# Kernel tuning notes

Hardware: AMD Instinct MI355X
Metric: run time of the kernel (lower is better)

Reference implementation:

```python
import jax, jax.numpy as jnp
import numpy as np

B, N, F, H = 256, 512, 256, 256
NUM_STAGES = 5
LN_EPS = 1e-5


def layer_norm(x, gamma, beta):
    m = jnp.mean(x, axis=-1, keepdims=True)
    v = jnp.mean((x - m) ** 2, axis=-1, keepdims=True)
    return (x - m) / jnp.sqrt(v + LN_EPS) * gamma + beta


def setup_inputs() -> dict:
    key = jax.random.key(0)
    ks = jax.random.split(key, 16)
    inp = {
        'adjacency': jax.random.normal(ks[0], (B, N, N), dtype=jnp.float32),
        'features': jax.random.normal(ks[1], (B, N, F), dtype=jnp.float32),
        'stage_ids': jax.random.randint(ks[2], (B, N), 0, NUM_STAGES, dtype=jnp.int32),
        # gc[0]: weight + bias
        'W0': jax.random.normal(ks[3], (F, H), dtype=jnp.float32) / np.sqrt(F),
        'b0': jax.random.normal(ks[4], (H,), dtype=jnp.float32) * 0.01,
        # gc[1]: bias only (weight=False)
        'b1': jax.random.normal(ks[5], (H,), dtype=jnp.float32) * 0.01,
        # gc[2]: weight + bias
        'W2': jax.random.normal(ks[6], (H, H), dtype=jnp.float32) / np.sqrt(H),
        'b2': jax.random.normal(ks[7], (H,), dtype=jnp.float32) * 0.01,
        # LayerNorm params (3 layers)
        'g0': jnp.ones((H,), jnp.float32), 'be0': jnp.zeros((H,), jnp.float32),
        'g1': jnp.ones((H,), jnp.float32), 'be1': jnp.zeros((H,), jnp.float32),
        'g2': jnp.ones((H,), jnp.float32), 'be2': jnp.zeros((H,), jnp.float32),
        # final fc: nhid -> 1
        'fcW': jax.random.normal(ks[8], (H, 1), dtype=jnp.float32) / np.sqrt(H),
        'fcb': jnp.zeros((1,), jnp.float32),
    }
    return inp


def reference(adjacency, features, stage_ids, W0, b0, b1, W2, b2,
              g0, be0, g1, be1, g2, be2, fcW, fcb):
    # --- layer 0: GraphConvolution(F->H) + LN + ReLU ---
    support = jnp.einsum('bnf,fh->bnh', features, W0)
    x = jnp.einsum('bnm,bmh->bnh', adjacency, support) + b0  # [B,N,H]
    x = jax.nn.relu(layer_norm(x, g0, be0))

    # --- layer 1: bias-add + ragged per-stage sum/argmax pooling ---
    out = x + b1                              # [B,N,H]
    scores = jnp.sum(out, axis=-1)            # [B,N] per-node row sums
    groups = jnp.arange(NUM_STAGES)
    in_group = stage_ids[:, None, :] == groups[None, :, None]  # [B,5,N]
    masked = jnp.where(in_group, scores[:, None, :], -jnp.inf)
    idx = jnp.argmax(masked, axis=-1)         # [B,5] best node per stage
    pooled = jnp.take_along_axis(out, idx[:, :, None], axis=1)  # [B,5,H]
    x = jax.nn.relu(layer_norm(pooled, g1, be1))

    # --- layer 2: GraphConvolution(H->H) with fixed 5x5 adjacency ---
    final_adj = jnp.zeros((NUM_STAGES, NUM_STAGES), x.dtype).at[0].set(1.0)
    support2 = jnp.einsum('bsh,hk->bsk', x, W2)
    x = jnp.einsum('ij,bjh->bih', final_adj, support2) + b2  # [B,5,H]
    x = jax.nn.relu(layer_norm(x, g2, be2))

    # --- head: fc(x[:, 0]) ---
    return x[:, 0] @ fcW + fcb                # [B,1]
```

## Files before the change

### kernel.cpp

```cpp
#include <hip/hip_runtime.h>
#include <stdint.h>

#define Bn 256
#define Nn 512
#define Fn 256
#define Hn 256
#define NSn 5
#define EPS 1e-5f
#define LSTR 56

typedef __attribute__((ext_vector_type(8))) short bf16x8;
typedef __attribute__((ext_vector_type(4))) float f32x4;

__device__ __forceinline__ unsigned short f2bf(float x) {
  unsigned int u = __float_as_uint(x);
  u += 0x7FFFu + ((u >> 16) & 1u);
  return (unsigned short)(u >> 16);
}
__device__ __forceinline__ unsigned int pack2bf(float a, float b) {
  return (unsigned int)f2bf(a) | ((unsigned int)f2bf(b) << 16);
}

__global__ __launch_bounds__(256) void k0_prep(const float* __restrict__ W0,
                                               unsigned short* __restrict__ W0T) {
  int idx = blockIdx.x * 256 + (int)threadIdx.x;
  int h = idx >> 8, f = idx & 255;
  W0T[h * Fn + f] = f2bf(W0[(size_t)f * Hn + h]);
}

__global__ __launch_bounds__(256) void k1_support(
    const float* __restrict__ feat, const unsigned short* __restrict__ W0T,
    unsigned short* __restrict__ supT)
{
  __shared__ __align__(16) unsigned short As[64 * LSTR];
  __shared__ __align__(16) unsigned short Bs[256 * LSTR];
  const int tid = (int)threadIdx.x;
  const int wv = tid >> 6, lane = tid & 63;
  const int m0 = blockIdx.x * 64;
  f32x4 acc[4][4];
  const f32x4 z4 = {0.f, 0.f, 0.f, 0.f};
#pragma unroll
  for (int i = 0; i < 4; ++i)
#pragma unroll
    for (int j = 0; j < 4; ++j) acc[i][j] = z4;

  const int ar = tid >> 2, ac = tid & 3;
  for (int k0 = 0; k0 < Fn; k0 += 32) {
    const float* ap = feat + (size_t)(m0 + ar) * Fn + k0 + ac * 4;
    float4 v0 = *(const float4*)ap;
    float4 v1 = *(const float4*)(ap + 16);
    *(uint2*)&As[ar * LSTR + ac * 4] =
        make_uint2(pack2bf(v0.x, v0.y), pack2bf(v0.z, v0.w));
    *(uint2*)&As[ar * LSTR + 16 + ac * 4] =
        make_uint2(pack2bf(v1.x, v1.y), pack2bf(v1.z, v1.w));
#pragma unroll
    for (int q = 0; q < 4; ++q) {
      int s = q * 256 + tid;
      int h = s >> 2, c = s & 3;
      *(uint4*)&Bs[h * LSTR + c * 8] =
          *(const uint4*)(W0T + (size_t)h * Fn + k0 + c * 8);
    }
    __syncthreads();
    bf16x8 af[4], bfr[4];
#pragma unroll
    for (int i = 0; i < 4; ++i) {
      af[i]  = *(const bf16x8*)&As[(i * 16 + (lane & 15)) * LSTR + (lane >> 4) * 8];
      bfr[i] = *(const bf16x8*)&Bs[(wv * 64 + i * 16 + (lane & 15)) * LSTR + (lane >> 4) * 8];
    }
#pragma unroll
    for (int mi = 0; mi < 4; ++mi)
#pragma unroll
      for (int nt = 0; nt < 4; ++nt)
        acc[mi][nt] = __builtin_amdgcn_mfma_f32_16x16x32_bf16(af[mi], bfr[nt], acc[mi][nt], 0, 0, 0);
    __syncthreads();
  }
  const int b = m0 >> 9;
  const int nodebase = m0 & 511;
  unsigned short* outb = supT + ((size_t)b << 17);
#pragma unroll
  for (int mi = 0; mi < 4; ++mi)
#pragma unroll
    for (int nt = 0; nt < 4; ++nt) {
      int h = wv * 64 + nt * 16 + (lane & 15);
      int node = nodebase + mi * 16 + (lane >> 4) * 4;
      *(uint2*)(outb + (size_t)h * Nn + node) =
          make_uint2(pack2bf(acc[mi][nt][0], acc[mi][nt][1]),
                     pack2bf(acc[mi][nt][2], acc[mi][nt][3]));
    }
}

__global__ __launch_bounds__(256) void k2_scores(
    const float* __restrict__ adj, const unsigned short* __restrict__ supT,
    const float* __restrict__ b0, const float* __restrict__ g0,
    const float* __restrict__ be0, float* __restrict__ scores)
{
  __shared__ __align__(16) unsigned short As[64 * LSTR];
  __shared__ __align__(16) unsigned short Bs[256 * LSTR];
  const int tid = (int)threadIdx.x;
  const int wv = tid >> 6, lane = tid & 63;
  const int b = blockIdx.x & 255;
  const int m0 = (blockIdx.x >> 8) * 64;
  const float* adjb = adj + ((size_t)b << 18);
  const unsigned short* supb = supT + ((size_t)b << 17);
  f32x4 acc[4][4];
  const f32x4 z4 = {0.f, 0.f, 0.f, 0.f};
#pragma unroll
  for (int i = 0; i < 4; ++i)
#pragma unroll
    for (int j = 0; j < 4; ++j) acc[i][j] = z4;

  const int ar = tid >> 2, ac = tid & 3;
  for (int k0 = 0; k0 < Nn; k0 += 32) {
    const float* ap = adjb + (size_t)(m0 + ar) * Nn + k0 + ac * 4;
    float4 v0 = *(const float4*)ap;
    float4 v1 = *(const float4*)(ap + 16);
    *(uint2*)&As[ar * LSTR + ac * 4] =
        make_uint2(pack2bf(v0.x, v0.y), pack2bf(v0.z, v0.w));
    *(uint2*)&As[ar * LSTR + 16 + ac * 4] =
        make_uint2(pack2bf(v1.x, v1.y), pack2bf(v1.z, v1.w));
#pragma unroll
    for (int q = 0; q < 4; ++q) {
      int s = q * 256 + tid;
      int h = s >> 2, c = s & 3;
      *(uint4*)&Bs[h * LSTR + c * 8] =
          *(const uint4*)(supb + (size_t)h * Nn + k0 + c * 8);
    }
    __syncthreads();
    bf16x8 af[4], bfr[4];
#pragma unroll
    for (int i = 0; i < 4; ++i) {
      af[i]  = *(const bf16x8*)&As[(i * 16 + (lane & 15)) * LSTR + (lane >> 4) * 8];
      bfr[i] = *(const bf16x8*)&Bs[(wv * 64 + i * 16 + (lane & 15)) * LSTR + (lane >> 4) * 8];
    }
#pragma unroll
    for (int mi = 0; mi < 4; ++mi)
#pragma unroll
      for (int nt = 0; nt < 4; ++nt)
        acc[mi][nt] = __builtin_amdgcn_mfma_f32_16x16x32_bf16(af[mi], bfr[nt], acc[mi][nt], 0, 0, 0);
    __syncthreads();
  }

  float* red = (float*)As;
  float b0v[4], g0v[4], be0v[4];
#pragma unroll
  for (int nt = 0; nt < 4; ++nt) {
    int col = wv * 64 + nt * 16 + (lane & 15);
    b0v[nt] = b0[col]; g0v[nt] = g0[col]; be0v[nt] = be0[col];
  }
#pragma unroll
  for (int mi = 0; mi < 4; ++mi)
#pragma unroll
    for (int rg = 0; rg < 4; ++rg) {
      float s1 = 0.f, s2 = 0.f;
#pragma unroll
      for (int nt = 0; nt < 4; ++nt) {
        float x = acc[mi][nt][rg] + b0v[nt];
        s1 += x; s2 += x * x;
      }
#pragma unroll
      for (int off = 8; off >= 1; off >>= 1) {
        s1 += __shfl_xor(s1, off);
        s2 += __shfl_xor(s2, off);
      }
      if ((lane & 15) == 0) {
        int row = mi * 16 + (lane >> 4) * 4 + rg;
        red[row * 4 + wv] = s1;
        red[256 + row * 4 + wv] = s2;
      }
    }
  __syncthreads();
#pragma unroll
  for (int mi = 0; mi < 4; ++mi)
#pragma unroll
    for (int rg = 0; rg < 4; ++rg) {
      int row = mi * 16 + (lane >> 4) * 4 + rg;
      float s1 = red[row*4] + red[row*4+1] + red[row*4+2] + red[row*4+3];
      float s2 = red[256+row*4] + red[256+row*4+1] + red[256+row*4+2] + red[256+row*4+3];
      float m = s1 * (1.0f / Hn);
      float var = s2 * (1.0f / Hn) - m * m;
      float rstd = 1.0f / sqrtf(var + EPS);
      float sc = 0.f;
#pragma unroll
      for (int nt = 0; nt < 4; ++nt) {
        float x = acc[mi][nt][rg] + b0v[nt];
        float zz = (x - m) * rstd * g0v[nt] + be0v[nt];
        sc += fmaxf(zz, 0.f);
      }
#pragma unroll
      for (int off = 8; off >= 1; off >>= 1) sc += __shfl_xor(sc, off);
      if ((lane & 15) == 0) red[512 + row * 4 + wv] = sc;
    }
  __syncthreads();
  if (tid < 64) {
    float s = red[512+tid*4] + red[512+tid*4+1] + red[512+tid*4+2] + red[512+tid*4+3];
    scores[b * Nn + m0 + tid] = s;
  }
}

__device__ __forceinline__ float brs(float v) {
  __shared__ float sb[4];
#pragma unroll
  for (int off = 32; off >= 1; off >>= 1) v += __shfl_xor(v, off);
  __syncthreads();
  if ((threadIdx.x & 63) == 0) sb[threadIdx.x >> 6] = v;
  __syncthreads();
  return sb[0] + sb[1] + sb[2] + sb[3];
}

__global__ __launch_bounds__(256) void k3_final(
    const float* __restrict__ adj, const float* __restrict__ feat,
    const float* __restrict__ scores, const int* __restrict__ sid,
    const float* __restrict__ W0, const float* __restrict__ b0,
    const float* __restrict__ b1, const float* __restrict__ W2,
    const float* __restrict__ b2, const float* __restrict__ g0,
    const float* __restrict__ be0, const float* __restrict__ g1,
    const float* __restrict__ be1, const float* __restrict__ g2,
    const float* __restrict__ be2, const float* __restrict__ fcW,
    const float* __restrict__ fcb, float* __restrict__ out)
{
  __shared__ float sc_s[Nn];
  __shared__ int sid_s[Nn];
  __shared__ __align__(16) float tT[Fn][20];
  __shared__ float xb[20][Hn];
  __shared__ unsigned long long redk[4];
  __shared__ int cand[20];
  __shared__ int candv[20];
  __shared__ float cm[20], cr[20], csc[20];
  __shared__ float xs[Hn];
  __shared__ int winslot[NSn];
  const int tid = (int)threadIdx.x;
  const int b = blockIdx.x;

  for (int i = tid; i < Nn; i += 256) {
    sc_s[i] = scores[b * Nn + i];
    sid_s[i] = sid[b * Nn + i];
  }
  __syncthreads();

  for (int s = 0; s < NSn; ++s) {
    for (int j = 0; j < 4; ++j) {
      unsigned long long best = 0ull;
      for (int i = tid; i < Nn; i += 256) {
        if (sid_s[i] == s) {
          unsigned int fbt = __float_as_uint(sc_s[i]);
          fbt = (fbt & 0x80000000u) ? ~fbt : (fbt | 0x80000000u);
          unsigned long long key = ((unsigned long long)fbt << 32) |
                                   (unsigned long long)(unsigned)(Nn - 1 - i);
          if (key > best) best = key;
        }
      }
#pragma unroll
      for (int off = 32; off >= 1; off >>= 1) {
        unsigned long long o = __shfl_xor(best, off);
        if (o > best) best = o;
      }
      __syncthreads();
      if ((tid & 63) == 0) redk[tid >> 6] = best;
      __syncthreads();
      best = redk[0];
      if (redk[1] > best) best = redk[1];
      if (redk[2] > best) best = redk[2];
      if (redk[3] > best) best = redk[3];
      if (tid == 0) {
        int c = s * 4 + j;
        if (best != 0ull) {
          int node = Nn - 1 - (int)(best & 0xFFFFFFFFull);
          cand[c] = node; candv[c] = 1; sid_s[node] = -1;
        } else {
          cand[c] = 0; candv[c] = 0;
        }
      }
      __syncthreads();
    }
  }

  const float* adjb = adj + ((size_t)b << 18);
  const float* fp = feat + ((size_t)b << 17) + tid;
  const float* ar[20];
#pragma unroll
  for (int c = 0; c < 20; ++c) {
    int row = __builtin_amdgcn_readfirstlane(cand[c]);
    ar[c] = adjb + ((size_t)row << 9);
  }
  double tacc[20];
#pragma unroll
  for (int c = 0; c < 20; ++c) tacc[c] = 0.0;
#pragma unroll 4
  for (int n = 0; n < Nn; ++n) {
    double v = (double)fp[(size_t)n << 8];
#pragma unroll
    for (int c = 0; c < 20; ++c) tacc[c] = fma((double)ar[c][n], v, tacc[c]);
  }
#pragma unroll
  for (int c = 0; c < 20; ++c) tT[tid][c] = (float)tacc[c];
  __syncthreads();

  double xc[20];
#pragma unroll
  for (int c = 0; c < 20; ++c) xc[c] = 0.0;
  const float* wp = W0 + tid;
  for (int f = 0; f < Fn; ++f) {
    double w = (double)wp[(size_t)f << 8];
    float4 t0 = *(const float4*)&tT[f][0];
    float4 t1 = *(const float4*)&tT[f][4];
    float4 t2 = *(const float4*)&tT[f][8];
    float4 t3 = *(const float4*)&tT[f][12];
    float4 t4 = *(const float4*)&tT[f][16];
    xc[0]  = fma((double)t0.x, w, xc[0]);   xc[1]  = fma((double)t0.y, w, xc[1]);
    xc[2]  = fma((double)t0.z, w, xc[2]);   xc[3]  = fma((double)t0.w, w, xc[3]);
    xc[4]  = fma((double)t1.x, w, xc[4]);   xc[5]  = fma((double)t1.y, w, xc[5]);
    xc[6]  = fma((double)t1.z, w, xc[6]);   xc[7]  = fma((double)t1.w, w, xc[7]);
    xc[8]  = fma((double)t2.x, w, xc[8]);   xc[9]  = fma((double)t2.y, w, xc[9]);
    xc[10] = fma((double)t2.z, w, xc[10]);  xc[11] = fma((double)t2.w, w, xc[11]);
    xc[12] = fma((double)t3.x, w, xc[12]);  xc[13] = fma((double)t3.y, w, xc[13]);
    xc[14] = fma((double)t3.z, w, xc[14]);  xc[15] = fma((double)t3.w, w, xc[15]);
    xc[16] = fma((double)t4.x, w, xc[16]);  xc[17] = fma((double)t4.y, w, xc[17]);
    xc[18] = fma((double)t4.z, w, xc[18]);  xc[19] = fma((double)t4.w, w, xc[19]);
  }
#pragma unroll
  for (int c = 0; c < 20; ++c) xb[c][tid] = (float)xc[c];
  __syncthreads();

  const float b0t = b0[tid], g0t = g0[tid], be0t = be0[tid];
  for (int c = 0; c < 20; ++c) {
    float xv = xb[c][tid] + b0t;
    float m = brs(xv) * (1.0f / Hn);
    float d = xv - m;
    float var = brs(d * d) * (1.0f / Hn);
    float rstd = 1.0f / sqrtf(var + EPS);
    float zz = d * rstd * g0t + be0t;
    float sc = brs(fmaxf(zz, 0.f));
    if (tid == 0) { cm[c] = m; cr[c] = rstd; csc[c] = sc; }
  }
  __syncthreads();

  if (tid == 0) {
#pragma unroll
    for (int s = 0; s < NSn; ++s) {
      int wsl = s * 4;
      float bestv = 0.f; int bestn = 0; bool any = false;
      for (int j = 0; j < 4; ++j) {
        int c = s * 4 + j;
        if (!candv[c]) continue;
        float v = csc[c]; int node = cand[c];
        if (!any || v > bestv || (v == bestv && node < bestn)) {
          any = true; bestv = v; bestn = node; wsl = c;
        }
      }
      winslot[s] = wsl;
    }
  }
  __syncthreads();

  const float b1t = b1[tid], g1t = g1[tid], be1t = be1[tid];
  float xsum = 0.f;
  for (int s = 0; s < NSn; ++s) {
    int c = winslot[s];
    float xv = xb[c][tid] + b0t;
    float z0 = (xv - cm[c]) * cr[c] * g0t + be0t;
    float o = fmaxf(z0, 0.f) + b1t;
    float m1 = brs(o) * (1.0f / Hn);
    float d1 = o - m1;
    float v1 = brs(d1 * d1) * (1.0f / Hn);
    float z1 = d1 * (1.0f / sqrtf(v1 + EPS)) * g1t + be1t;
    xsum += fmaxf(z1, 0.f);
  }
  xs[tid] = xsum;
  __syncthreads();
  float y = 0.f;
  for (int h = 0; h < Hn; h += 4) {
    float4 xv4 = *(const float4*)&xs[h];
    y = fmaf(xv4.x, W2[(size_t)h * Hn + tid], y);
    y = fmaf(xv4.y, W2[(size_t)(h + 1) * Hn + tid], y);
    y = fmaf(xv4.z, W2[(size_t)(h + 2) * Hn + tid], y);
    y = fmaf(xv4.w, W2[(size_t)(h + 3) * Hn + tid], y);
  }
  y += b2[tid];
  float m2 = brs(y) * (1.0f / Hn);
  float d2 = y - m2;
  float v2 = brs(d2 * d2) * (1.0f / Hn);
  float z2 = d2 * (1.0f / sqrtf(v2 + EPS)) * g2[tid] + be2[tid];
  float p = fmaxf(z2, 0.f) * fcW[tid];
  float tot = brs(p);
  if (tid == 0) out[b] = tot + fcb[0];
}

extern "C" void kernel_launch(void* const* d_in, const int* in_sizes, int n_in,
                              void* d_out, int out_size, void* d_ws, size_t ws_size,
                              hipStream_t stream)
{
  (void)in_sizes; (void)n_in; (void)out_size; (void)ws_size;
  const float* adj  = (const float*)d_in[0];
  const float* feat = (const float*)d_in[1];
  const int*   sid  = (const int*)d_in[2];
  const float* W0   = (const float*)d_in[3];
  const float* b0   = (const float*)d_in[4];
  const float* b1   = (const float*)d_in[5];
  const float* W2   = (const float*)d_in[6];
  const float* b2   = (const float*)d_in[7];
  const float* g0   = (const float*)d_in[8];
  const float* be0  = (const float*)d_in[9];
  const float* g1   = (const float*)d_in[10];
  const float* be1  = (const float*)d_in[11];
  const float* g2   = (const float*)d_in[12];
  const float* be2  = (const float*)d_in[13];
  const float* fcW  = (const float*)d_in[14];
  const float* fcb  = (const float*)d_in[15];
  float* out = (float*)d_out;

  unsigned short* supT = (unsigned short*)d_ws;
  unsigned short* W0T  = (unsigned short*)((char*)d_ws + 67108864);
  float* scores        = (float*)((char*)d_ws + 67108864 + 131072);

  k0_prep<<<dim3(256), dim3(256), 0, stream>>>(W0, W0T);
  k1_support<<<dim3(2048), dim3(256), 0, stream>>>(feat, W0T, supT);
  k2_scores<<<dim3(2048), dim3(256), 0, stream>>>(adj, supT, b0, g0, be0, scores);
  k3_final<<<dim3(256), dim3(256), 0, stream>>>(adj, feat, scores, sid,
      W0, b0, b1, W2, b2, g0, be0, g1, be1, g2, be2, fcW, fcb, out);
}
```

Baseline: 866.8 us.

## Split final candidate recompute across node chunks and reduce in separate kernel

The per-batch final kernel is split in two. A 1024-block kernel selects the candidate nodes and computes partial adjacency-row times feature products over 128-node chunks, staging the adjacency rows in shared memory. A second kernel sums the four partials, runs the W0 projection in fp32 instead of fp64, and computes the candidate LayerNorms with one wave per candidate instead of block-wide reductions. The W0 transpose now goes through a shared-memory tile, and k2 block ordering groups all row tiles of one batch together. The trade-off is extra fp64 partial traffic through global memory and some loss of precision in the projection.

```diff
diff --git a/kernel.cpp b/kernel.cpp
--- a/kernel.cpp
+++ b/kernel.cpp
@@ -23,9 +23,27 @@
 
 __global__ __launch_bounds__(256) void k0_prep(const float* __restrict__ W0,
                                                unsigned short* __restrict__ W0T) {
-  int idx = blockIdx.x * 256 + (int)threadIdx.x;
-  int h = idx >> 8, f = idx & 255;
-  W0T[h * Fn + f] = f2bf(W0[(size_t)f * Hn + h]);
+  __shared__ float tile[64][68];
+  const int tid = (int)threadIdx.x;
+  const int ti = blockIdx.x >> 2, tj = blockIdx.x & 3;
+#pragma unroll
+  for (int q = 0; q < 4; ++q) {
+    int s = tid + 256 * q;
+    int r = s >> 4, c4 = s & 15;
+    *(float4*)&tile[r][c4 * 4] =
+        *(const float4*)(W0 + (size_t)(ti * 64 + r) * Hn + tj * 64 + c4 * 4);
+  }
+  __syncthreads();
+#pragma unroll
+  for (int q = 0; q < 4; ++q) {
+    int s = tid + 256 * q;
+    int hh = s >> 4, fq = s & 15;
+    int ff = fq * 4;
+    float t0 = tile[ff + 0][hh], t1 = tile[ff + 1][hh];
+    float t2 = tile[ff + 2][hh], t3 = tile[ff + 3][hh];
+    *(uint2*)(W0T + (size_t)(tj * 64 + hh) * Fn + ti * 64 + ff) =
+        make_uint2(pack2bf(t0, t1), pack2bf(t2, t3));
+  }
 }
 
 __global__ __launch_bounds__(256) void k1_support(
@@ -98,8 +116,8 @@
   __shared__ __align__(16) unsigned short Bs[256 * LSTR];
   const int tid = (int)threadIdx.x;
   const int wv = tid >> 6, lane = tid & 63;
-  const int b = blockIdx.x & 255;
-  const int m0 = (blockIdx.x >> 8) * 64;
+  const int b = blockIdx.x >> 3;
+  const int m0 = (blockIdx.x & 7) * 64;
   const float* adjb = adj + ((size_t)b << 18);
   const unsigned short* supb = supT + ((size_t)b << 17);
   f32x4 acc[4][4];
@@ -197,6 +215,92 @@
   }
 }
 
+__global__ __launch_bounds__(256) void k3b_part(
+    const float* __restrict__ adj, const float* __restrict__ feat,
+    const float* __restrict__ scores, const int* __restrict__ sid,
+    int* __restrict__ candbuf, double* __restrict__ px)
+{
+  __shared__ float sc_s[Nn];
+  __shared__ int sid_s[Nn];
+  __shared__ __align__(16) float adjs[20][128];
+  __shared__ unsigned long long redk[4];
+  __shared__ int cand[20], candv[20];
+  const int tid = (int)threadIdx.x;
+  const int b = blockIdx.x >> 2, ch = blockIdx.x & 3;
+
+  for (int i = tid; i < Nn; i += 256) {
+    sc_s[i] = scores[b * Nn + i];
+    sid_s[i] = sid[b * Nn + i];
+  }
+  __syncthreads();
+
+  for (int s = 0; s < NSn; ++s)
+    for (int j = 0; j < 4; ++j) {
+      unsigned long long best = 0ull;
+      for (int i = tid; i < Nn; i += 256)
+        if (sid_s[i] == s) {
+          unsigned int fb = __float_as_uint(sc_s[i]);
+          fb = (fb & 0x80000000u) ? ~fb : (fb | 0x80000000u);
+          unsigned long long key = ((unsigned long long)fb << 32) |
+                                   (unsigned long long)(unsigned)(Nn - 1 - i);
+          if (key > best) best = key;
+        }
+#pragma unroll
+      for (int off = 32; off >= 1; off >>= 1) {
+        unsigned long long o = __shfl_xor(best, off);
+        if (o > best) best = o;
+      }
+      if ((tid & 63) == 0) redk[tid >> 6] = best;
+      __syncthreads();
+      if (tid == 0) {
+        unsigned long long bb = redk[0];
+        if (redk[1] > bb) bb = redk[1];
+        if (redk[2] > bb) bb = redk[2];
+        if (redk[3] > bb) bb = redk[3];
+        int c = s * 4 + j;
+        if (bb != 0ull) {
+          int node = Nn - 1 - (int)(bb & 0xFFFFFFFFull);
+          cand[c] = node; candv[c] = 1; sid_s[node] = -1;
+        } else {
+          cand[c] = 0; candv[c] = 0;
+        }
+      }
+      __syncthreads();
+    }
+
+  if (ch == 0 && tid < 20) {
+    candbuf[b * 40 + tid] = cand[tid];
+    candbuf[b * 40 + 20 + tid] = candv[tid];
+  }
+
+  const float* adjb = adj + ((size_t)b << 18);
+  for (int idx = tid; idx < 20 * 128; idx += 256) {
+    int c = idx >> 7, n = idx & 127;
+    adjs[c][n] = adjb[((size_t)cand[c] << 9) + ch * 128 + n];
+  }
+  __syncthreads();
+
+  double t[20];
+#pragma unroll
+  for (int c = 0; c < 20; ++c) t[c] = 0.0;
+  const float* fp = feat + ((size_t)b << 17) + (((size_t)ch * 128) << 8) + tid;
+  for (int n0 = 0; n0 < 128; n0 += 4) {
+    double d0 = (double)fp[(size_t)(n0 + 0) << 8];
+    double d1 = (double)fp[(size_t)(n0 + 1) << 8];
+    double d2 = (double)fp[(size_t)(n0 + 2) << 8];
+    double d3 = (double)fp[(size_t)(n0 + 3) << 8];
+#pragma unroll
+    for (int c = 0; c < 20; ++c) {
+      float4 av = *(const float4*)&adjs[c][n0];
+      t[c] += (double)av.x * d0 + (double)av.y * d1 +
+              (double)av.z * d2 + (double)av.w * d3;
+    }
+  }
+  double* pxb = px + ((size_t)(b * 4 + ch) * 20) * 256 + tid;
+#pragma unroll
+  for (int c = 0; c < 20; ++c) pxb[(size_t)c * 256] = t[c];
+}
+
 __device__ __forceinline__ float brs(float v) {
   __shared__ float sb[4];
 #pragma unroll
@@ -207,9 +311,8 @@
   return sb[0] + sb[1] + sb[2] + sb[3];
 }
 
-__global__ __launch_bounds__(256) void k3_final(
-    const float* __restrict__ adj, const float* __restrict__ feat,
-    const float* __restrict__ scores, const int* __restrict__ sid,
+__global__ __launch_bounds__(256) void k3c_final(
+    const double* __restrict__ px, const int* __restrict__ candbuf,
     const float* __restrict__ W0, const float* __restrict__ b0,
     const float* __restrict__ b1, const float* __restrict__ W2,
     const float* __restrict__ b2, const float* __restrict__ g0,
@@ -218,119 +321,83 @@
     const float* __restrict__ be2, const float* __restrict__ fcW,
     const float* __restrict__ fcb, float* __restrict__ out)
 {
-  __shared__ float sc_s[Nn];
-  __shared__ int sid_s[Nn];
-  __shared__ __align__(16) float tT[Fn][20];
+  __shared__ __align__(16) float tfT[Fn * 20];
   __shared__ float xb[20][Hn];
-  __shared__ unsigned long long redk[4];
-  __shared__ int cand[20];
-  __shared__ int candv[20];
+  __shared__ float b0s[Hn], g0s[Hn], be0s[Hn];
   __shared__ float cm[20], cr[20], csc[20];
+  __shared__ int candL[20], candvL[20], winslot[NSn];
   __shared__ float xs[Hn];
-  __shared__ int winslot[NSn];
   const int tid = (int)threadIdx.x;
   const int b = blockIdx.x;
 
-  for (int i = tid; i < Nn; i += 256) {
-    sc_s[i] = scores[b * Nn + i];
-    sid_s[i] = sid[b * Nn + i];
-  }
-  __syncthreads();
-
-  for (int s = 0; s < NSn; ++s) {
-    for (int j = 0; j < 4; ++j) {
-      unsigned long long best = 0ull;
-      for (int i = tid; i < Nn; i += 256) {
-        if (sid_s[i] == s) {
-          unsigned int fbt = __float_as_uint(sc_s[i]);
-          fbt = (fbt & 0x80000000u) ? ~fbt : (fbt | 0x80000000u);
-          unsigned long long key = ((unsigned long long)fbt << 32) |
-                                   (unsigned long long)(unsigned)(Nn - 1 - i);
-          if (key > best) best = key;
-        }
-      }
-#pragma unroll
-      for (int off = 32; off >= 1; off >>= 1) {
-        unsigned long long o = __shfl_xor(best, off);
-        if (o > best) best = o;
-      }
-      __syncthreads();
-      if ((tid & 63) == 0) redk[tid >> 6] = best;
-      __syncthreads();
-      best = redk[0];
-      if (redk[1] > best) best = redk[1];
-      if (redk[2] > best) best = redk[2];
-      if (redk[3] > best) best = redk[3];
-      if (tid == 0) {
-        int c = s * 4 + j;
-        if (best != 0ull) {
-          int node = Nn - 1 - (int)(best & 0xFFFFFFFFull);
-          cand[c] = node; candv[c] = 1; sid_s[node] = -1;
-        } else {
-          cand[c] = 0; candv[c] = 0;
-        }
-      }
-      __syncthreads();
-    }
-  }
-
-  const float* adjb = adj + ((size_t)b << 18);
-  const float* fp = feat + ((size_t)b << 17) + tid;
-  const float* ar[20];
-#pragma unroll
-  for (int c = 0; c < 20; ++c) {
-    int row = __builtin_amdgcn_readfirstlane(cand[c]);
-    ar[c] = adjb + ((size_t)row << 9);
-  }
-  double tacc[20];
-#pragma unroll
-  for (int c = 0; c < 20; ++c) tacc[c] = 0.0;
-#pragma unroll 4
-  for (int n = 0; n < Nn; ++n) {
-    double v = (double)fp[(size_t)n << 8];
-#pragma unroll
-    for (int c = 0; c < 20; ++c) tacc[c] = fma((double)ar[c][n], v, tacc[c]);
-  }
-#pragma unroll
-  for (int c = 0; c < 20; ++c) tT[tid][c] = (float)tacc[c];
-  __syncthreads();
-
-  double xc[20];
-#pragma unroll
-  for (int c = 0; c < 20; ++c) xc[c] = 0.0;
-  const float* wp = W0 + tid;
-  for (int f = 0; f < Fn; ++f) {
-    double w = (double)wp[(size_t)f << 8];
-    float4 t0 = *(const float4*)&tT[f][0];
-    float4 t1 = *(const float4*)&tT[f][4];
-    float4 t2 = *(const float4*)&tT[f][8];
-    float4 t3 = *(const float4*)&tT[f][12];
-    float4 t4 = *(const float4*)&tT[f][16];
-    xc[0]  = fma((double)t0.x, w, xc[0]);   xc[1]  = fma((double)t0.y, w, xc[1]);
-    xc[2]  = fma((double)t0.z, w, xc[2]);   xc[3]  = fma((double)t0.w, w, xc[3]);
-    xc[4]  = fma((double)t1.x, w, xc[4]);   xc[5]  = fma((double)t1.y, w, xc[5]);
-    xc[6]  = fma((double)t1.z, w, xc[6]);   xc[7]  = fma((double)t1.w, w, xc[7]);
-    xc[8]  = fma((double)t2.x, w, xc[8]);   xc[9]  = fma((double)t2.y, w, xc[9]);
-    xc[10] = fma((double)t2.z, w, xc[10]);  xc[11] = fma((double)t2.w, w, xc[11]);
-    xc[12] = fma((double)t3.x, w, xc[12]);  xc[13] = fma((double)t3.y, w, xc[13]);
-    xc[14] = fma((double)t3.z, w, xc[14]);  xc[15] = fma((double)t3.w, w, xc[15]);
-    xc[16] = fma((double)t4.x, w, xc[16]);  xc[17] = fma((double)t4.y, w, xc[17]);
-    xc[18] = fma((double)t4.z, w, xc[18]);  xc[19] = fma((double)t4.w, w, xc[19]);
-  }
-#pragma unroll
-  for (int c = 0; c < 20; ++c) xb[c][tid] = (float)xc[c];
-  __syncthreads();
-
-  const float b0t = b0[tid], g0t = g0[tid], be0t = be0[tid];
-  for (int c = 0; c < 20; ++c) {
-    float xv = xb[c][tid] + b0t;
-    float m = brs(xv) * (1.0f / Hn);
-    float d = xv - m;
-    float var = brs(d * d) * (1.0f / Hn);
-    float rstd = 1.0f / sqrtf(var + EPS);
-    float zz = d * rstd * g0t + be0t;
-    float sc = brs(fmaxf(zz, 0.f));
-    if (tid == 0) { cm[c] = m; cr[c] = rstd; csc[c] = sc; }
+  if (tid < 20) {
+    candL[tid] = candbuf[b * 40 + tid];
+    candvL[tid] = candbuf[b * 40 + 20 + tid];
+  }
+  b0s[tid] = b0[tid]; g0s[tid] = g0[tid]; be0s[tid] = be0[tid];
+  {
+    const double* pxb = px + ((size_t)b * 4 * 20) * 256 + tid;
+#pragma unroll
+    for (int c = 0; c < 20; ++c) {
+      double t = pxb[(size_t)c * 256] + pxb[(size_t)(20 + c) * 256] +
+                 pxb[(size_t)(40 + c) * 256] + pxb[(size_t)(60 + c) * 256];
+      tfT[tid * 20 + c] = (float)t;
+    }
+  }
+  __syncthreads();
+
+  {
+    float xc[20];
+#pragma unroll
+    for (int c = 0; c < 20; ++c) xc[c] = 0.f;
+    for (int f = 0; f < Fn; ++f) {
+      float w = W0[(size_t)f * Hn + tid];
+      const float* tp = &tfT[f * 20];
+      float4 t0 = *(const float4*)(tp);
+      float4 t1 = *(const float4*)(tp + 4);
+      float4 t2 = *(const float4*)(tp + 8);
+      float4 t3 = *(const float4*)(tp + 12);
+      float4 t4 = *(const float4*)(tp + 16);
+      xc[0] = fmaf(t0.x, w, xc[0]);   xc[1] = fmaf(t0.y, w, xc[1]);
+      xc[2] = fmaf(t0.z, w, xc[2]);   xc[3] = fmaf(t0.w, w, xc[3]);
+      xc[4] = fmaf(t1.x, w, xc[4]);   xc[5] = fmaf(t1.y, w, xc[5]);
+      xc[6] = fmaf(t1.z, w, xc[6]);   xc[7] = fmaf(t1.w, w, xc[7]);
+      xc[8] = fmaf(t2.x, w, xc[8]);   xc[9] = fmaf(t2.y, w, xc[9]);
+      xc[10] = fmaf(t2.z, w, xc[10]); xc[11] = fmaf(t2.w, w, xc[11]);
+      xc[12] = fmaf(t3.x, w, xc[12]); xc[13] = fmaf(t3.y, w, xc[13]);
+      xc[14] = fmaf(t3.z, w, xc[14]); xc[15] = fmaf(t3.w, w, xc[15]);
+      xc[16] = fmaf(t4.x, w, xc[16]); xc[17] = fmaf(t4.y, w, xc[17]);
+      xc[18] = fmaf(t4.z, w, xc[18]); xc[19] = fmaf(t4.w, w, xc[19]);
+    }
+#pragma unroll
+    for (int c = 0; c < 20; ++c) xb[c][tid] = xc[c];
+  }
+  __syncthreads();
+
+  {
+    const int wv = tid >> 6, lane = tid & 63;
+    for (int c = wv; c < 20; c += 4) {
+      float v0 = xb[c][lane] + b0s[lane];
+      float v1 = xb[c][lane + 64] + b0s[lane + 64];
+      float v2 = xb[c][lane + 128] + b0s[lane + 128];
+      float v3 = xb[c][lane + 192] + b0s[lane + 192];
+      float s = v0 + v1 + v2 + v3;
+#pragma unroll
+      for (int off = 32; off >= 1; off >>= 1) s += __shfl_xor(s, off);
+      float m = s * (1.0f / Hn);
+      float d0 = v0 - m, d1 = v1 - m, d2 = v2 - m, d3 = v3 - m;
+      float s2 = d0 * d0 + d1 * d1 + d2 * d2 + d3 * d3;
+#pragma unroll
+      for (int off = 32; off >= 1; off >>= 1) s2 += __shfl_xor(s2, off);
+      float rstd = 1.0f / sqrtf(s2 * (1.0f / Hn) + EPS);
+      float sc = fmaxf(d0 * rstd * g0s[lane] + be0s[lane], 0.f) +
+                 fmaxf(d1 * rstd * g0s[lane + 64] + be0s[lane + 64], 0.f) +
+                 fmaxf(d2 * rstd * g0s[lane + 128] + be0s[lane + 128], 0.f) +
+                 fmaxf(d3 * rstd * g0s[lane + 192] + be0s[lane + 192], 0.f);
+#pragma unroll
+      for (int off = 32; off >= 1; off >>= 1) sc += __shfl_xor(sc, off);
+      if (lane == 0) { cm[c] = m; cr[c] = rstd; csc[c] = sc; }
+    }
   }
   __syncthreads();
 
@@ -341,8 +408,8 @@
       float bestv = 0.f; int bestn = 0; bool any = false;
       for (int j = 0; j < 4; ++j) {
         int c = s * 4 + j;
-        if (!candv[c]) continue;
-        float v = csc[c]; int node = cand[c];
+        if (!candvL[c]) continue;
+        float v = csc[c]; int node = candL[c];
         if (!any || v > bestv || (v == bestv && node < bestn)) {
           any = true; bestv = v; bestn = node; wsl = c;
         }
@@ -352,6 +419,7 @@
   }
   __syncthreads();
 
+  const float b0t = b0s[tid], g0t = g0s[tid], be0t = be0s[tid];
   const float b1t = b1[tid], g1t = g1[tid], be1t = be1[tid];
   float xsum = 0.f;
   for (int s = 0; s < NSn; ++s) {
@@ -410,11 +478,14 @@
 
   unsigned short* supT = (unsigned short*)d_ws;
   unsigned short* W0T  = (unsigned short*)((char*)d_ws + 67108864);
-  float* scores        = (float*)((char*)d_ws + 67108864 + 131072);
-
-  k0_prep<<<dim3(256), dim3(256), 0, stream>>>(W0, W0T);
+  float* scores        = (float*)((char*)d_ws + 67239936);
+  int* candbuf         = (int*)((char*)d_ws + 67764224);
+  double* px           = (double*)((char*)d_ws + 67805184);
+
+  k0_prep<<<dim3(16), dim3(256), 0, stream>>>(W0, W0T);
   k1_support<<<dim3(2048), dim3(256), 0, stream>>>(feat, W0T, supT);
   k2_scores<<<dim3(2048), dim3(256), 0, stream>>>(adj, supT, b0, g0, be0, scores);
-  k3_final<<<dim3(256), dim3(256), 0, stream>>>(adj, feat, scores, sid,
+  k3b_part<<<dim3(1024), dim3(256), 0, stream>>>(adj, feat, scores, sid, candbuf, px);
+  k3c_final<<<dim3(256), dim3(256), 0, stream>>>(px, candbuf,
       W0, b0, b1, W2, b2, g0, be0, g1, be1, g2, be2, fcW, fcb, out);
 }
```

Result: faster. 738.2 us (-14.8%).
